# Performance work log

Measured on AMD Instinct MI355X. Metric: run time of the kernel, lower is better.

Reference implementation:

```python
import jax, jax.numpy as jnp
import numpy as np

# H36M 17-joint skeleton: parent-of array
_PARENTS = [-1, 0, 1, 2, 0, 4, 5, 0, 7, 8, 9, 8, 11, 12, 8, 14, 15]

def _make_triplets():
    # (jp, j, jc) for every joint j with a parent jp and child jc
    trips = []
    for jc, j in enumerate(_PARENTS):
        if j <= 0 and j != 0:
            continue
        if j == -1:
            continue
        jp = _PARENTS[j]
        if jp == -1:
            continue
        trips.append((jp, j, jc))
    return trips

TRIPLETS = _make_triplets()  # 12 fixed triplets

B, N, J, C = 16, 243, 17, 512
H, D = 8, C // 8
EPS = 1e-5


def setup_inputs() -> dict:
    key = jax.random.key(0)
    ks = jax.random.split(key, 5)
    s = 1.0 / np.sqrt(C)
    x = jax.random.normal(ks[0], (B, N, J, C), dtype=jnp.float32)
    Wqkv = jax.random.normal(ks[1], (C, 3 * C), dtype=jnp.float32) * s
    bqkv = jax.random.normal(ks[2], (3 * C,), dtype=jnp.float32) * 0.01
    Wproj = jax.random.normal(ks[3], (C, C), dtype=jnp.float32) * s
    bproj = jax.random.normal(ks[4], (C,), dtype=jnp.float32) * 0.01
    return {"x": x, "Wqkv": Wqkv, "bqkv": bqkv, "Wproj": Wproj, "bproj": bproj}


def _hsdm(x, Wqkv, bqkv, Wproj, bproj):
    # x: (B, N, J, C) -> tokens over joints per frame
    xf = x.reshape(B * N, J, C)
    qkv = xf @ Wqkv + bqkv                                   # (BN, J, 3C)
    qkv = qkv.reshape(B * N, J, 3, H, D).transpose(2, 0, 3, 1, 4)  # (3, BN, H, J, D)
    q, k, v = qkv[0], qkv[1], qkv[2]
    scale = 1.0 / jnp.sqrt(jnp.float32(D))
    attn = jax.nn.softmax(jnp.einsum('bhqd,bhkd->bhqk', q, k) * scale, axis=-1)
    # sequential hierarchical adjustment over fixed skeleton triplets
    # (order matters: later triplets read entries written by earlier ones)
    for jp, j, jc in TRIPLETS:
        half = attn[:, :, j, jp] * 0.5
        attn = attn.at[:, :, j, jc].add(half).at[:, :, jc, j].add(half)
    # dropout is identity at inference
    xa = jnp.einsum('bhqk,bhkd->bhqd', attn, v)              # (BN, H, J, D)
    xa = xa.transpose(0, 2, 1, 3).reshape(B * N, J, C)
    xa = xa @ Wproj + bproj
    y = x + xa.reshape(B, N, J, C)
    mu = jnp.mean(y, axis=-1, keepdims=True)
    var = jnp.var(y, axis=-1, keepdims=True)
    return (y - mu) / jnp.sqrt(var + EPS)                     # LN without affine


def reference(x, Wqkv, bqkv, Wproj, bproj):
    return _hsdm(x, Wqkv, bqkv, Wproj, bproj)
```

## Files before the change

### kernel.cpp

```cpp
#include <hip/hip_runtime.h>

typedef unsigned short u16;
typedef unsigned int u32;
typedef short bf16x8 __attribute__((ext_vector_type(8)));
typedef float f32x4 __attribute__((ext_vector_type(4)));
typedef float f32x16 __attribute__((ext_vector_type(16)));

#define M_ROWS   66096
#define M_PAD    66176
#define C_DIM    512
#define NQKV     1536
#define NFRAME   3888


__device__ __forceinline__ u16 f2bf(float f) {
    u32 u = __float_as_uint(f);
    u32 r = (u + 0x7fffu + ((u >> 16) & 1u)) >> 16;
    return (u16)r;
}
__device__ __forceinline__ float bf2f(u16 v) {
    return __uint_as_float(((u32)v) << 16);
}
__device__ __forceinline__ void async16(const void* g, void* l) {
    __builtin_amdgcn_global_load_lds(
        (const __attribute__((address_space(1))) unsigned int*)g,
        (__attribute__((address_space(3))) unsigned int*)l, 16, 0, 0);
}


__global__ __launch_bounds__(256) void cast_x(const float* __restrict__ x, u16* __restrict__ xb) {
    u32 cid = blockIdx.x * 256u + threadIdx.x;
    u32 m  = cid >> 6;
    u32 c0 = (cid & 63u) * 8u;
    if (m >= M_PAD) return;
    u16 v[8];
    if (m < M_ROWS) {
        const float* p = x + (size_t)m * C_DIM + c0;
        float4 f1 = *(const float4*)p;
        float4 f2 = *(const float4*)(p + 4);
        v[0]=f2bf(f1.x); v[1]=f2bf(f1.y); v[2]=f2bf(f1.z); v[3]=f2bf(f1.w);
        v[4]=f2bf(f2.x); v[5]=f2bf(f2.y); v[6]=f2bf(f2.z); v[7]=f2bf(f2.w);
    } else {
        #pragma unroll
        for (int i = 0; i < 8; ++i) v[i] = 0;
    }
    u16* dst = xb + ((size_t)(c0 >> 5) * M_PAD + m) * 32 + (c0 & 31u);
    *(uint4*)dst = *(const uint4*)v;
}


__global__ __launch_bounds__(256) void cast_w(const float* __restrict__ W, u16* __restrict__ out, int N) {
    __shared__ float tile[32 * 65];
    const int n0 = blockIdx.x * 64;
    const int kt = blockIdx.y;
    const int t  = threadIdx.x;
    for (int i = t; i < 2048; i += 256) {
        int k = i >> 6, n = i & 63;
        tile[k * 65 + n] = W[(size_t)(kt * 32 + k) * N + n0 + n];
    }
    __syncthreads();
    {
        int n = t >> 2, kk0 = (t & 3) * 8;
        u16 v[8];
        #pragma unroll
        for (int j = 0; j < 8; ++j) v[j] = f2bf(tile[(kk0 + j) * 65 + n]);
        u16* dst = out + ((size_t)kt * N + n0 + n) * 32 + kk0;
        *(uint4*)dst = *(const uint4*)v;
    }
}


__global__ __launch_bounds__(256) void gemm1(const u16* __restrict__ xb,
                                             const u16* __restrict__ wt,
                                             const float* __restrict__ bqkv,
                                             u16* __restrict__ qkv) {
    __shared__ u16 As[2][128 * 32];
    __shared__ u16 Bs[2][128 * 32];
    __shared__ float biasS[128];

    const int n0 = blockIdx.x * 128;
    const int m0 = blockIdx.y * 128;
    const int t  = threadIdx.x;
    const int w  = t >> 6, l = t & 63;
    const int lr = l & 15, lq = l >> 4;
    const int wr = (w >> 1) * 64, wc = (w & 1) * 64;

    if (t < 128) biasS[t] = bqkv[n0 + t];

    f32x4 acc[4][4] = {};

    auto stage = [&](int kt, int bi) {
        const u16* ga = xb + ((size_t)kt * M_PAD + m0) * 32;
        const u16* gb = wt + ((size_t)kt * NQKV + n0) * 32;
        async16(ga + (size_t)t * 8,         &As[bi][t * 8]);
        async16(ga + (size_t)(t + 256) * 8, &As[bi][(t + 256) * 8]);
        async16(gb + (size_t)t * 8,         &Bs[bi][t * 8]);
        async16(gb + (size_t)(t + 256) * 8, &Bs[bi][(t + 256) * 8]);
    };

    stage(0, 0);
    __syncthreads();

    for (int kt = 0; kt < 16; ++kt) {
        const int cur = kt & 1;
        if (kt < 15) stage(kt + 1, cur ^ 1);

        bf16x8 a[4], b[4];
        #pragma unroll
        for (int i = 0; i < 4; ++i) a[i] = *(const bf16x8*)&As[cur][(wr + i * 16 + lr) * 32 + lq * 8];
        #pragma unroll
        for (int i = 0; i < 4; ++i) b[i] = *(const bf16x8*)&Bs[cur][(wc + i * 16 + lr) * 32 + lq * 8];
        #pragma unroll
        for (int i = 0; i < 4; ++i)
            #pragma unroll
            for (int j = 0; j < 4; ++j)
                acc[i][j] = __builtin_amdgcn_mfma_f32_16x16x32_bf16(a[i], b[j], acc[i][j], 0, 0, 0);

        __syncthreads();
    }

    #pragma unroll
    for (int i = 0; i < 4; ++i) {
        #pragma unroll
        for (int j = 0; j < 4; ++j) {
            const int col  = n0 + wc + j * 16 + lr;
            const float bb = biasS[wc + j * 16 + lr];
            #pragma unroll
            for (int r = 0; r < 4; ++r) {
                const int row = m0 + wr + i * 16 + lq * 4 + r;
                if (row < M_ROWS)
                    qkv[(size_t)row * NQKV + col] = f2bf(acc[i][j][r] + bb);
            }
        }
    }
}


__global__ __launch_bounds__(256) void attn_k(const u16* __restrict__ qkv, u16* __restrict__ xa) {
    __shared__ u16 Pb[4][32 * 40];

    const int wv  = threadIdx.x >> 6;
    const int l   = threadIdx.x & 63;
    const int l31 = l & 31;
    const int hi  = l >> 5;

    const int id = blockIdx.x * 4 + wv;
    const int f  = id >> 3;
    const int h  = id & 7;

    const int mrow = (l31 < 17) ? l31 : 0;
    const u16* base = qkv + (size_t)(f * 17) * NQKV;
    const u16* Qp = base + (size_t)mrow * NQKV + h * 64 + 8 * hi;
    const u16* Kp = Qp + 512;

    f32x16 Sacc = {};
    #pragma unroll
    for (int c = 0; c < 4; ++c) {
        bf16x8 aq = *(const bf16x8*)(Qp + 16 * c);
        bf16x8 bk = *(const bf16x8*)(Kp + 16 * c);
        Sacc = __builtin_amdgcn_mfma_f32_32x32x16_bf16(aq, bk, Sacc, 0, 0, 0);
    }

    float p[16];
    #pragma unroll
    for (int r = 0; r < 16; ++r)
        p[r] = (l31 < 17) ? Sacc[r] * 0.125f : -1e30f;

    #pragma unroll
    for (int r = 0; r < 16; ++r) {
        float mx = p[r];
        #pragma unroll
        for (int m = 1; m < 32; m <<= 1) mx = fmaxf(mx, __shfl_xor(mx, m));
        float e = __expf(p[r] - mx);
        float s = e;
        #pragma unroll
        for (int m = 1; m < 32; m <<= 1) s += __shfl_xor(s, m);
        p[r] = e * __builtin_amdgcn_rcpf(s);
    }

    {
        constexpr int TJP[13] = {0,1,0,4,0,7,8,7,8,11,7,8,14};
        constexpr int TJ [13] = {1,2,4,5,7,8,9,8,11,12,8,14,15};
        constexpr int TJC[13] = {2,3,5,6,8,9,10,11,12,13,14,15,16};
        #pragma unroll
        for (int tr = 0; tr < 13; ++tr) {
            const int jp = TJP[tr], j = TJ[tr], jc = TJC[tr];
            const int rj = (j  & 3) | ((j  >> 3) << 2), hj = (j  >> 2) & 1;
            const int rc = (jc & 3) | ((jc >> 3) << 2), hc = (jc >> 2) & 1;
            const float half = 0.5f * __shfl(p[rj], jp + 32 * hj);
            if (l == jc + 32 * hj) p[rj] += half;
            if (l == j  + 32 * hc) p[rc] += half;
        }
    }

    u16* Pw = Pb[wv];
    #pragma unroll
    for (int r = 0; r < 16; ++r) {
        const int row = (r & 3) + 8 * (r >> 2) + 4 * hi;
        Pw[row * 40 + l31] = f2bf(p[r]);
    }
    asm volatile("s_waitcnt lgkmcnt(0)" ::: "memory");

    bf16x8 pa[2];
    #pragma unroll
    for (int c = 0; c < 2; ++c)
        pa[c] = *(const bf16x8*)&Pw[l31 * 40 + 16 * c + 8 * hi];

    const u16* Vbase = base + 1024 + h * 64;
    f32x16 O[2] = {};
    #pragma unroll
    for (int t = 0; t < 2; ++t) {
        #pragma unroll
        for (int c = 0; c < 2; ++c) {
            u16 vv[8];
            #pragma unroll
            for (int j = 0; j < 8; ++j) {
                const int k  = 16 * c + 8 * hi + j;
                const int kr = (k < 17) ? k : 0;
                vv[j] = Vbase[(size_t)kr * NQKV + t * 32 + l31];
            }
            O[t] = __builtin_amdgcn_mfma_f32_32x32x16_bf16(pa[c], *(const bf16x8*)vv, O[t], 0, 0, 0);
        }
    }

    #pragma unroll
    for (int t = 0; t < 2; ++t) {
        const int kt = h * 2 + t;
        #pragma unroll
        for (int r = 0; r < 16; ++r) {
            const int row = (r & 3) + 8 * (r >> 2) + 4 * hi;
            if (row < 17)
                xa[((size_t)kt * M_PAD + (f * 17 + row)) * 32 + l31] = f2bf(O[t][r]);
        }
    }
}


#define G2_LOAD(kt, Af, Bf)                                                          \
    {                                                                                \
        const u16* ga = xa + ((size_t)(kt) * M_PAD + m0 + lr) * 32 + lq * 8;         \
        const u16* gb = wt + ((size_t)(kt) * C_DIM + wn * 64 + lr) * 32 + lq * 8;    \
        _Pragma("unroll") for (int i = 0; i < 8; ++i)                                \
            Af[i] = *(const bf16x8*)(ga + (size_t)i * 512);                          \
        _Pragma("unroll") for (int j = 0; j < 4; ++j)                                \
            Bf[j] = *(const bf16x8*)(gb + (size_t)j * 512);                          \
    }

#define G2_MFMA(Af, Bf)                                                              \
    _Pragma("unroll") for (int i = 0; i < 8; ++i)                                    \
        _Pragma("unroll") for (int j = 0; j < 4; ++j)                                \
            acc[i][j] = __builtin_amdgcn_mfma_f32_16x16x32_bf16(Af[i], Bf[j], acc[i][j], 0, 0, 0);

__global__ __launch_bounds__(512, 2) void gemm2_ln(const u16* __restrict__ xa,
                                                   const u16* __restrict__ wt,
                                                   const float* __restrict__ bproj,
                                                   const float* __restrict__ x,
                                                   float* __restrict__ out) {
    __shared__ float partS[128][9];
    __shared__ float partQ[128][9];

    const int m0 = blockIdx.x * 128;
    const int t  = threadIdx.x;
    const int wn = t >> 6, l = t & 63;
    const int lr = l & 15, lq = l >> 4;

    f32x4 acc[8][4] = {};
    bf16x8 A0[8], B0[4], A1[8], B1[4];

    G2_LOAD(0, A0, B0);
    #pragma unroll 1
    for (int kt = 0; kt < 14; kt += 2) {
        G2_LOAD(kt + 1, A1, B1);
        G2_MFMA(A0, B0);
        G2_LOAD(kt + 2, A0, B0);
        G2_MFMA(A1, B1);
    }
    G2_LOAD(15, A1, B1);
    G2_MFMA(A0, B0);
    G2_MFMA(A1, B1);

    float bias_[4];
    #pragma unroll
    for (int j = 0; j < 4; ++j) bias_[j] = bproj[wn * 64 + j * 16 + lr];

    #pragma unroll
    for (int i = 0; i < 8; ++i) {
        #pragma unroll
        for (int rr = 0; rr < 4; ++rr) {
            const int rl   = i * 16 + lq * 4 + rr;
            const int rowg = m0 + rl;
            const bool valid = rowg < M_ROWS;
            const float* xr = x + (size_t)rowg * C_DIM + wn * 64 + lr;
            float s = 0.f, q = 0.f;
            #pragma unroll
            for (int j = 0; j < 4; ++j) {
                float v = acc[i][j][rr] + bias_[j];
                if (valid) v += xr[j * 16];
                acc[i][j][rr] = v;
                s += v;
                q += v * v;
            }
            #pragma unroll
            for (int m = 1; m < 16; m <<= 1) {
                s += __shfl_xor(s, m);
                q += __shfl_xor(q, m);
            }
            if (lr == 0) {
                partS[rl][wn] = s;
                partQ[rl][wn] = q;
            }
        }
    }
    __syncthreads();

    if (t < 128) {
        float ss = 0.f, qq = 0.f;
        #pragma unroll
        for (int w2 = 0; w2 < 8; ++w2) { ss += partS[t][w2]; qq += partQ[t][w2]; }
        const float mean = ss * (1.f / 512.f);
        const float var  = qq * (1.f / 512.f) - mean * mean;
        partS[t][8] = mean;
        partQ[t][8] = rsqrtf(var + 1e-5f);
    }
    __syncthreads();

    #pragma unroll
    for (int i = 0; i < 8; ++i) {
        #pragma unroll
        for (int rr = 0; rr < 4; ++rr) {
            const int rl   = i * 16 + lq * 4 + rr;
            const int rowg = m0 + rl;
            if (rowg < M_ROWS) {
                const float mean = partS[rl][8];
                const float rstd = partQ[rl][8];
                float* orow = out + (size_t)rowg * C_DIM + wn * 64 + lr;
                #pragma unroll
                for (int j = 0; j < 4; ++j)
                    orow[j * 16] = (acc[i][j][rr] - mean) * rstd;
            }
        }
    }
}


extern "C" void kernel_launch(void* const* d_in, const int* in_sizes, int n_in,
                              void* d_out, int out_size, void* d_ws, size_t ws_size,
                              hipStream_t stream) {
    const float* x     = (const float*)d_in[0];
    const float* Wqkv  = (const float*)d_in[1];
    const float* bqkv  = (const float*)d_in[2];
    const float* Wproj = (const float*)d_in[3];
    const float* bproj = (const float*)d_in[4];
    float* out = (float*)d_out;

    u16* xb  = (u16*)d_ws;
    u16* wqt = xb  + (size_t)M_PAD * C_DIM;
    u16* wpt = wqt + (size_t)NQKV * C_DIM;
    u16* qkv = wpt + (size_t)C_DIM * C_DIM;
    u16* xa  = qkv + (size_t)M_PAD * NQKV;

    cast_x<<<(M_PAD * 64) / 256, 256, 0, stream>>>(x, xb);
    cast_w<<<dim3(NQKV / 64, 16), 256, 0, stream>>>(Wqkv, wqt, NQKV);
    cast_w<<<dim3(C_DIM / 64, 16), 256, 0, stream>>>(Wproj, wpt, C_DIM);
    gemm1<<<dim3(NQKV / 128, M_PAD / 128), 256, 0, stream>>>(xb, wqt, bqkv, qkv);
    attn_k<<<(NFRAME * 8) / 4, 256, 0, stream>>>(qkv, xa);
    gemm2_ln<<<(M_PAD / 128), 512, 0, stream>>>(xa, wpt, bproj, x, out);
}
```

Baseline: 698.8 us.

## Stage gemm2 tiles through double-buffered LDS with async loads and halve row tile

The projection+LayerNorm GEMM now copies A and B tiles into double-buffered shared memory with async global-to-LDS loads, instead of having each wave read its fragments straight from global memory into registers. The row tile drops from 128 to 64 rows, which doubles the grid, cuts the accumulator registers, and raises the launch-bounds occupancy hint. This aims to remove redundant global reads of the weight tile across waves and to improve latency hiding. The cost is a barrier every k-step, and the full 512-column B tile is reloaded for every 64-row block, so weight traffic doubles per output row.

Result: faster. 631.2 us (-9.7%).

```diff
diff --git a/kernel.cpp b/kernel.cpp
--- a/kernel.cpp
+++ b/kernel.cpp
@@ -236,55 +236,59 @@
 }
 
 
-#define G2_LOAD(kt, Af, Bf)                                                          \
-    {                                                                                \
-        const u16* ga = xa + ((size_t)(kt) * M_PAD + m0 + lr) * 32 + lq * 8;         \
-        const u16* gb = wt + ((size_t)(kt) * C_DIM + wn * 64 + lr) * 32 + lq * 8;    \
-        _Pragma("unroll") for (int i = 0; i < 8; ++i)                                \
-            Af[i] = *(const bf16x8*)(ga + (size_t)i * 512);                          \
-        _Pragma("unroll") for (int j = 0; j < 4; ++j)                                \
-            Bf[j] = *(const bf16x8*)(gb + (size_t)j * 512);                          \
-    }
-
-#define G2_MFMA(Af, Bf)                                                              \
-    _Pragma("unroll") for (int i = 0; i < 8; ++i)                                    \
-        _Pragma("unroll") for (int j = 0; j < 4; ++j)                                \
-            acc[i][j] = __builtin_amdgcn_mfma_f32_16x16x32_bf16(Af[i], Bf[j], acc[i][j], 0, 0, 0);
-
-__global__ __launch_bounds__(512, 2) void gemm2_ln(const u16* __restrict__ xa,
+__global__ __launch_bounds__(512, 4) void gemm2_ln(const u16* __restrict__ xa,
                                                    const u16* __restrict__ wt,
                                                    const float* __restrict__ bproj,
                                                    const float* __restrict__ x,
                                                    float* __restrict__ out) {
-    __shared__ float partS[128][9];
-    __shared__ float partQ[128][9];
-
-    const int m0 = blockIdx.x * 128;
+    __shared__ u16 As[2][64 * 32];
+    __shared__ u16 Bs[2][512 * 32];
+    __shared__ float partS[64][9];
+    __shared__ float partQ[64][9];
+
+    const int m0 = blockIdx.x * 64;
     const int t  = threadIdx.x;
     const int wn = t >> 6, l = t & 63;
     const int lr = l & 15, lq = l >> 4;
 
-    f32x4 acc[8][4] = {};
-    bf16x8 A0[8], B0[4], A1[8], B1[4];
-
-    G2_LOAD(0, A0, B0);
-    #pragma unroll 1
-    for (int kt = 0; kt < 14; kt += 2) {
-        G2_LOAD(kt + 1, A1, B1);
-        G2_MFMA(A0, B0);
-        G2_LOAD(kt + 2, A0, B0);
-        G2_MFMA(A1, B1);
-    }
-    G2_LOAD(15, A1, B1);
-    G2_MFMA(A0, B0);
-    G2_MFMA(A1, B1);
+    f32x4 acc[4][4] = {};
+
+    auto stage = [&](int kt, int bi) {
+        const u16* ga = xa + ((size_t)kt * M_PAD + m0) * 32;
+        const u16* gb = wt + ((size_t)kt * C_DIM) * 32;
+        if (t < 256) async16(ga + (size_t)t * 8, &As[bi][t * 8]);
+        #pragma unroll
+        for (int i = 0; i < 4; ++i)
+            async16(gb + (size_t)(t + 512 * i) * 8, &Bs[bi][(t + 512 * i) * 8]);
+    };
+
+    stage(0, 0);
+    __syncthreads();
+
+    for (int kt = 0; kt < 16; ++kt) {
+        const int cur = kt & 1;
+        if (kt < 15) stage(kt + 1, cur ^ 1);
+
+        bf16x8 a[4], b[4];
+        #pragma unroll
+        for (int i = 0; i < 4; ++i) a[i] = *(const bf16x8*)&As[cur][(i * 16 + lr) * 32 + lq * 8];
+        #pragma unroll
+        for (int j = 0; j < 4; ++j) b[j] = *(const bf16x8*)&Bs[cur][(wn * 64 + j * 16 + lr) * 32 + lq * 8];
+        #pragma unroll
+        for (int i = 0; i < 4; ++i)
+            #pragma unroll
+            for (int j = 0; j < 4; ++j)
+                acc[i][j] = __builtin_amdgcn_mfma_f32_16x16x32_bf16(a[i], b[j], acc[i][j], 0, 0, 0);
+
+        __syncthreads();
+    }
 
     float bias_[4];
     #pragma unroll
     for (int j = 0; j < 4; ++j) bias_[j] = bproj[wn * 64 + j * 16 + lr];
 
     #pragma unroll
-    for (int i = 0; i < 8; ++i) {
+    for (int i = 0; i < 4; ++i) {
         #pragma unroll
         for (int rr = 0; rr < 4; ++rr) {
             const int rl   = i * 16 + lq * 4 + rr;
@@ -313,7 +317,7 @@
     }
     __syncthreads();
 
-    if (t < 128) {
+    if (t < 64) {
         float ss = 0.f, qq = 0.f;
         #pragma unroll
         for (int w2 = 0; w2 < 8; ++w2) { ss += partS[t][w2]; qq += partQ[t][w2]; }
@@ -325,7 +329,7 @@
     __syncthreads();
 
     #pragma unroll
-    for (int i = 0; i < 8; ++i) {
+    for (int i = 0; i < 4; ++i) {
         #pragma unroll
         for (int rr = 0; rr < 4; ++rr) {
             const int rl   = i * 16 + lq * 4 + rr;
@@ -364,5 +368,5 @@
     cast_w<<<dim3(C_DIM / 64, 16), 256, 0, stream>>>(Wproj, wpt, C_DIM);
     gemm1<<<dim3(NQKV / 128, M_PAD / 128), 256, 0, stream>>>(xb, wqt, bqkv, qkv);
     attn_k<<<(NFRAME * 8) / 4, 256, 0, stream>>>(qkv, xa);
-    gemm2_ln<<<(M_PAD / 128), 512, 0, stream>>>(xa, wpt, bproj, x, out);
-}
+    gemm2_ln<<<(M_PAD / 64), 512, 0, stream>>>(xa, wpt, bproj, x, out);
+}
```
